# Kernel optimization log

Hardware: AMD Instinct MI355X
Metric: run time of the kernel (lower is better)

Reference implementation:

```python
import jax, jax.numpy as jnp
import numpy as np

N, E = 50000, 1600000
F_IN, F_EDGE, HID = 128, 16, 64
SLOPE = 0.2
EPS_BN = 1e-5


def setup_inputs() -> dict:
    key = jax.random.key(0)
    ks = jax.random.split(key, 24)
    g = lambda k, shp, s=0.1: (jax.random.normal(k, shp, dtype=jnp.float32) * s)
    inp = {
        'x': jax.random.normal(ks[0], (N, F_IN), dtype=jnp.float32),
        'edge_index': jax.random.randint(ks[1], (2, E), 0, N, dtype=jnp.int64),
        'edge_attr': jax.random.normal(ks[2], (E, F_EDGE), dtype=jnp.float32),
        # conv1: F_IN -> HID, 4 heads, concat
        'W1': g(ks[3], (F_IN, 4 * HID)), 'a1s': g(ks[4], (4, HID)), 'a1d': g(ks[5], (4, HID)), 'b1': jnp.zeros((4 * HID,), jnp.float32),
        # conv2: 4*HID -> HID, 4 heads, concat
        'W2': g(ks[6], (4 * HID, 4 * HID)), 'a2s': g(ks[7], (4, HID)), 'a2d': g(ks[8], (4, HID)), 'b2': jnp.zeros((4 * HID,), jnp.float32),
        # conv3: 4*HID -> HID, 1 head
        'W3': g(ks[9], (4 * HID, HID)), 'a3s': g(ks[10], (1, HID)), 'a3d': g(ks[11], (1, HID)), 'b3': jnp.zeros((HID,), jnp.float32),
        'bn1_g': jnp.ones((4 * HID,), jnp.float32), 'bn1_b': jnp.zeros((4 * HID,), jnp.float32),
        'bn2_g': jnp.ones((4 * HID,), jnp.float32), 'bn2_b': jnp.zeros((4 * HID,), jnp.float32),
        'mlp_W1': g(ks[12], (F_EDGE, HID)), 'mlp_b1': jnp.zeros((HID,), jnp.float32),
        'mlp_W2': g(ks[13], (HID, HID)), 'mlp_b2': jnp.zeros((HID,), jnp.float32),
        'fc_W': g(ks[14], (3 * HID, 1)), 'fc_b': jnp.zeros((1,), jnp.float32),
    }
    return inp


def _gat(x, W, a_s, a_d, b, src, dst, heads, dout):
    n = x.shape[0]
    h = (x @ W).reshape(n, heads, dout)                    # [N,H,D]
    ls = jnp.sum(h * a_s, axis=-1)                         # [N,H]
    ld = jnp.sum(h * a_d, axis=-1)
    logits = jax.nn.leaky_relu(ls[src] + ld[dst], SLOPE)   # [E',H]
    m = jax.ops.segment_max(logits, dst, num_segments=n)
    m = jnp.where(jnp.isfinite(m), m, 0.0)
    p = jnp.exp(logits - m[dst])
    s = jax.ops.segment_sum(p, dst, num_segments=n)
    alpha = p / (s[dst] + 1e-16)                           # segment softmax over in-edges
    out = jax.ops.segment_sum(h[src] * alpha[:, :, None], dst, num_segments=n)
    return out.reshape(n, heads * dout) + b


def _bn(x, g, b):
    mu = jnp.mean(x, axis=0)
    var = jnp.var(x, axis=0)
    return (x - mu) * jax.lax.rsqrt(var + EPS_BN) * g + b


def reference(x, edge_index, edge_attr, W1, a1s, a1d, b1, W2, a2s, a2d, b2,
              W3, a3s, a3d, b3, bn1_g, bn1_b, bn2_g, bn2_b,
              mlp_W1, mlp_b1, mlp_W2, mlp_b2, fc_W, fc_b):
    src0, dst0 = edge_index[0], edge_index[1]
    loop = jnp.arange(x.shape[0], dtype=edge_index.dtype)  # PyG adds self-loops
    src = jnp.concatenate([src0, loop])
    dst = jnp.concatenate([dst0, loop])

    h = _gat(x, W1, a1s, a1d, b1, src, dst, 4, HID)
    h = _bn(jax.nn.elu(h), bn1_g, bn1_b)
    h = _gat(h, W2, a2s, a2d, b2, src, dst, 4, HID)
    h = _bn(jax.nn.elu(h), bn2_g, bn2_b)
    h = _gat(h, W3, a3s, a3d, b3, src, dst, 1, HID)        # [N,HID]

    ef = jax.nn.relu(edge_attr @ mlp_W1 + mlp_b1) @ mlp_W2 + mlp_b2  # [E,HID]
    emb = jnp.concatenate([h[src0], h[dst0], ef], axis=1)  # [E,3*HID]
    return (emb @ fc_W + fc_b).squeeze(-1)
```

## Files before the change

### kernel.cpp

```cpp
#include <hip/hip_runtime.h>
#include <hip/hip_fp16.h>
#include <math.h>


#define FIN 128
#define HID 64
#define BIN_SHIFT 8

typedef _Float16 f16x8 __attribute__((ext_vector_type(8)));
typedef float f32x4 __attribute__((ext_vector_type(4)));

__device__ __forceinline__ unsigned short f2hbits(float f) {
    __half h = __float2half(f);
    return *reinterpret_cast<unsigned short*>(&h);
}
__device__ __forceinline__ float2 hpair(unsigned w) {
    __half2 h = *reinterpret_cast<__half2*>(&w);
    return __half22float2(h);
}

__device__ __forceinline__ unsigned fenc(float f) {
    unsigned b = __float_as_uint(f);
    return (b & 0x80000000u) ? ~b : (b | 0x80000000u);
}
__device__ __forceinline__ float fdec(unsigned k) {
    unsigned b = (k & 0x80000000u) ? (k ^ 0x80000000u) : ~k;
    return __uint_as_float(b);
}


__global__ __launch_bounds__(256) void bincount_kernel(const int* __restrict__ ei,
                                                       int* __restrict__ bincnt,
                                                       int E, int Etot) {
    __shared__ int h[256];
    int t = threadIdx.x;
    h[t] = 0;
    __syncthreads();
    int base = blockIdx.x * 4096;
    #pragma unroll
    for (int i = 0; i < 16; ++i) {
        int e = base + i * 256 + t;
        if (e < Etot) {
            int d = (e < E) ? ei[E + e] : (e - E);
            atomicAdd(&h[d >> BIN_SHIFT], 1);
        }
    }
    __syncthreads();
    if (h[t]) atomicAdd(&bincnt[t], h[t]);
}

__global__ void scanbins_kernel(const int* __restrict__ bincnt, int* __restrict__ binptr,
                                int* __restrict__ bincur, int NB, int Etot) {
    __shared__ int buf[256];
    int t = threadIdx.x;
    int v = (t < NB) ? bincnt[t] : 0;
    buf[t] = v;
    __syncthreads();
    for (int o = 1; o < 256; o <<= 1) {
        int y = (t >= o) ? buf[t - o] : 0;
        __syncthreads();
        buf[t] += y;
        __syncthreads();
    }
    int excl = buf[t] - v;
    if (t < NB) {
        binptr[t] = excl;
        bincur[t] = excl;
    }
    if (t == 0) binptr[NB] = Etot;
}

__global__ __launch_bounds__(256) void binscatter_kernel(const int* __restrict__ ei,
                                                         int* __restrict__ bincur,
                                                         int2* __restrict__ binned,
                                                         int E, int Etot) {
    __shared__ int h[256];
    __shared__ int gb[256];
    int t = threadIdx.x;
    h[t] = 0;
    __syncthreads();
    int base = blockIdx.x * 4096;
    #pragma unroll
    for (int i = 0; i < 16; ++i) {
        int e = base + i * 256 + t;
        if (e < Etot) {
            int d = (e < E) ? ei[E + e] : (e - E);
            atomicAdd(&h[d >> BIN_SHIFT], 1);
        }
    }
    __syncthreads();
    int cnt = h[t];
    if (cnt) gb[t] = atomicAdd(&bincur[t], cnt);
    __syncthreads();
    h[t] = 0;
    __syncthreads();
    #pragma unroll
    for (int i = 0; i < 16; ++i) {
        int e = base + i * 256 + t;
        if (e < Etot) {
            int s, d;
            if (e < E) { s = ei[e]; d = ei[E + e]; }
            else       { s = e - E; d = e - E; }
            int b = d >> BIN_SHIFT;
            int pos = gb[b] + atomicAdd(&h[b], 1);
            binned[pos] = make_int2(s, d);
        }
    }
}

__global__ __launch_bounds__(256) void bincsr_kernel(const int2* __restrict__ binned,
                                                     const int* __restrict__ binptr,
                                                     int* __restrict__ row_ptr,
                                                     int* __restrict__ col,
                                                     int N, int Etot) {
    __shared__ int h[256];
    __shared__ int cur[256];
    __shared__ int wsum[4];
    int b = blockIdx.x;
    int t = threadIdx.x;
    int lo = b << BIN_SHIFT;
    h[t] = 0;
    __syncthreads();
    int ebeg = binptr[b], eend = binptr[b + 1];
    for (int i = ebeg + t; i < eend; i += 256) atomicAdd(&h[binned[i].y - lo], 1);
    __syncthreads();
    int v = h[t];
    int lane = t & 63, w = t >> 6;
    int x = v;
    #pragma unroll
    for (int o = 1; o < 64; o <<= 1) {
        int y = __shfl_up(x, o);
        if (lane >= o) x += y;
    }
    if (lane == 63) wsum[w] = x;
    __syncthreads();
    int off = 0;
    #pragma unroll
    for (int i = 0; i < 4; ++i) off += (i < w) ? wsum[i] : 0;
    int excl = ebeg + off + x - v;
    int node = lo + t;
    if (node < N) row_ptr[node] = excl;
    cur[t] = excl;
    if (b == 0 && t == 0) row_ptr[N] = Etot;
    __syncthreads();
    for (int i = ebeg + t; i < eend; i += 256) {
        int2 sd = binned[i];
        int pos = atomicAdd(&cur[sd.y - lo], 1);
        col[pos] = sd.x;
    }
}


__global__ __launch_bounds__(256) void mfma_gemm_kernel(
    const float* __restrict__ X, const float* __restrict__ W,
    unsigned short* __restrict__ Yh, int Nrows, int K, int M,
    const float* __restrict__ bnsum, const float* __restrict__ bng,
    const float* __restrict__ bnb, float invN,
    const float* __restrict__ as_, const float* __restrict__ ad_,
    float* __restrict__ ls, float* __restrict__ ld,
    unsigned* __restrict__ lsmax_g, int H) {
    __shared__ __align__(16) unsigned short a_lds[128][40];
    __shared__ __align__(16) unsigned short b_lds[64][40];
    __shared__ __align__(16) float scale_l[256];
    __shared__ __align__(16) float shift_l[256];
    __shared__ unsigned lmax_l;
    const int t = threadIdx.x;
    const int nrt = (Nrows + 127) >> 7;
    int rowt, by;
    if (H == 4) {
        int idx = blockIdx.x;
        by = (idx >> 3) & 3;
        rowt = (idx & 7) + (idx >> 5) * 8;
        if (rowt >= nrt) return;
    } else {
        by = 0;
        rowt = blockIdx.x;
    }
    const int row0 = rowt * 128;
    const int c0 = by * 64;
    const int w = t >> 6, lane = t & 63;
    const int quad = lane >> 4, mrow = lane & 15;
    if (t == 0) lmax_l = 0;
    if (bnsum && t < 256) {
        float mu = bnsum[t] * invN;
        float var = bnsum[256 + t] * invN - mu * mu;
        float sc = bng[t] * rsqrtf(var + 1e-5f);
        scale_l[t] = sc;
        shift_l[t] = bnb[t] - mu * sc;
    }
    __syncthreads();
    const unsigned short* X16 = (const unsigned short*)X;
    f32x4 acc[2][4] = {};
    for (int k0 = 0; k0 < K; k0 += 32) {
        #pragma unroll
        for (int i = 0; i < 4; ++i) {
            int f = i * 256 + t;
            int r = f >> 3, kq = f & 7;
            int grow = row0 + r;
            float4 xv = make_float4(0.f, 0.f, 0.f, 0.f);
            if (bnsum) {
                uint2 hw = make_uint2(0u, 0u);
                if (grow < Nrows)
                    hw = *(const uint2*)(X16 + (size_t)grow * K + k0 + kq * 4);
                float2 f01 = hpair(hw.x), f23 = hpair(hw.y);
                xv = make_float4(f01.x, f01.y, f23.x, f23.y);
                float4 sc = *(const float4*)&scale_l[k0 + kq * 4];
                float4 sh = *(const float4*)&shift_l[k0 + kq * 4];
                xv.x = fmaf(xv.x, sc.x, sh.x);
                xv.y = fmaf(xv.y, sc.y, sh.y);
                xv.z = fmaf(xv.z, sc.z, sh.z);
                xv.w = fmaf(xv.w, sc.w, sh.w);
            } else {
                if (grow < Nrows)
                    xv = *(const float4*)(X + (size_t)grow * K + k0 + kq * 4);
            }
            ushort4 pk;
            pk.x = f2hbits(xv.x);
            pk.y = f2hbits(xv.y);
            pk.z = f2hbits(xv.z);
            pk.w = f2hbits(xv.w);
            *(ushort4*)&a_lds[r][kq * 4] = pk;
        }
        #pragma unroll
        for (int i = 0; i < 2; ++i) {
            int f = i * 256 + t;
            int kr = f >> 4, cq = f & 15;
            float4 wv = *(const float4*)(W + (size_t)(k0 + kr) * M + c0 + cq * 4);
            b_lds[cq * 4 + 0][kr] = f2hbits(wv.x);
            b_lds[cq * 4 + 1][kr] = f2hbits(wv.y);
            b_lds[cq * 4 + 2][kr] = f2hbits(wv.z);
            b_lds[cq * 4 + 3][kr] = f2hbits(wv.w);
        }
        __syncthreads();
        f16x8 a0 = *(const f16x8*)&a_lds[w * 32 + mrow][quad * 8];
        f16x8 a1 = *(const f16x8*)&a_lds[w * 32 + 16 + mrow][quad * 8];
        #pragma unroll
        for (int c = 0; c < 4; ++c) {
            f16x8 bf = *(const f16x8*)&b_lds[c * 16 + mrow][quad * 8];
            acc[0][c] = __builtin_amdgcn_mfma_f32_16x16x32_f16(a0, bf, acc[0][c], 0, 0, 0);
            acc[1][c] = __builtin_amdgcn_mfma_f32_16x16x32_f16(a1, bf, acc[1][c], 0, 0, 0);
        }
        __syncthreads();
    }
    #pragma unroll
    for (int i = 0; i < 2; ++i) {
        #pragma unroll
        for (int c = 0; c < 4; ++c) {
            #pragma unroll
            for (int r = 0; r < 4; ++r) {
                int grow = row0 + w * 32 + i * 16 + quad * 4 + r;
                if (grow < Nrows)
                    Yh[(size_t)grow * M + c0 + c * 16 + mrow] = f2hbits(acc[i][c][r]);
            }
        }
    }
    float asv[4], adv[4];
    #pragma unroll
    for (int c = 0; c < 4; ++c) {
        asv[c] = as_[by * 64 + c * 16 + mrow];
        adv[c] = ad_[by * 64 + c * 16 + mrow];
    }
    float lmax = -3.0e38f;
    #pragma unroll
    for (int i = 0; i < 2; ++i) {
        #pragma unroll
        for (int r = 0; r < 4; ++r) {
            float ps = 0.f, pd = 0.f;
            #pragma unroll
            for (int c = 0; c < 4; ++c) {
                ps = fmaf(acc[i][c][r], asv[c], ps);
                pd = fmaf(acc[i][c][r], adv[c], pd);
            }
            #pragma unroll
            for (int o = 1; o <= 8; o <<= 1) {
                ps += __shfl_xor(ps, o);
                pd += __shfl_xor(pd, o);
            }
            int grow = row0 + w * 32 + i * 16 + quad * 4 + r;
            if (mrow == 0 && grow < Nrows) {
                ls[(size_t)grow * H + by] = ps;
                ld[(size_t)grow * H + by] = pd;
                lmax = fmaxf(lmax, ps);
            }
        }
    }
    if (mrow == 0) atomicMax(&lmax_l, fenc(lmax));
    __syncthreads();
    if (t == 0) atomicMax(&lsmax_g[by], lmax_l);
}


#define ACC8(hv, p)                                              \
    {                                                            \
        float2 fa = hpair((hv).x), fb = hpair((hv).y);           \
        float2 fc = hpair((hv).z), fd = hpair((hv).w);           \
        a0 = fmaf((p), fa.x, a0); a1 = fmaf((p), fa.y, a1);      \
        a2 = fmaf((p), fb.x, a2); a3 = fmaf((p), fb.y, a3);      \
        a4 = fmaf((p), fc.x, a4); a5 = fmaf((p), fc.y, a5);      \
        a6 = fmaf((p), fd.x, a6); a7 = fmaf((p), fd.y, a7);      \
    }

__global__ __launch_bounds__(256) void agg_bn_kernel(
    const unsigned short* __restrict__ hb, const float* __restrict__ ls,
    const float* __restrict__ ld, const int* __restrict__ row_ptr,
    const int* __restrict__ col, const float* __restrict__ bias,
    const unsigned* __restrict__ lsmax_g, unsigned short* __restrict__ out,
    float* __restrict__ bnsum, int N, int ngroups) {
    __shared__ float accs[4][256];
    __shared__ float accq[4][256];
    const int t = threadIdx.x;
    const int w = t >> 6, lane = t & 63;
    const int half = lane >> 5;
    const int il = lane & 31;
    const int hd = il >> 3;
    const int c0 = il * 8;
    const char* hbb = (const char*)hb;
    const char* lsc = (const char*)ls;
    const unsigned cb = (unsigned)c0 * 2u;
    const unsigned hd4 = (unsigned)hd * 4u;
    if (half == 0) {
        #pragma unroll
        for (int i = 0; i < 8; ++i) { accs[w][c0 + i] = 0.f; accq[w][c0 + i] = 0.f; }
    }
    const float lsm = fdec(lsmax_g[hd]);
    const float4 bv0 = *(const float4*)(bias + c0);
    const float4 bv1 = *(const float4*)(bias + c0 + 4);
    for (int g = blockIdx.x; g < ngroups; g += gridDim.x) {
        int n = g * 4 + w;
        if (n >= N) continue;
        int beg = row_ptr[n], end = row_ptr[n + 1];
        float4 ldn = *(const float4*)(ld + (size_t)n * 4);
        float ldn_h = (hd == 0) ? ldn.x : (hd == 1) ? ldn.y : (hd == 2) ? ldn.z : ldn.w;
        float m_h = fmaxf(0.f, ldn_h + lsm);
        float psum = 0.f;
        float a0 = 0.f, a1 = 0.f, a2 = 0.f, a3 = 0.f;
        float a4 = 0.f, a5 = 0.f, a6 = 0.f, a7 = 0.f;
        for (int base = beg; base < end; base += 64) {
            int el = base + lane;
            int s_r = (el < end) ? col[el] : 0;
            int cnt = min(64, end - base);
            int j = 0;
            for (; j + 8 <= cnt; j += 8) {
                int s0 = __shfl(s_r, j + half);
                int s1 = __shfl(s_r, j + 2 + half);
                int s2 = __shfl(s_r, j + 4 + half);
                int s3 = __shfl(s_r, j + 6 + half);
                uint4 h0 = *(const uint4*)(hbb + ((unsigned)s0 * 512u + cb));
                uint4 h1 = *(const uint4*)(hbb + ((unsigned)s1 * 512u + cb));
                uint4 h2 = *(const uint4*)(hbb + ((unsigned)s2 * 512u + cb));
                uint4 h3 = *(const uint4*)(hbb + ((unsigned)s3 * 512u + cb));
                float l0 = *(const float*)(lsc + ((unsigned)s0 * 16u + hd4));
                float l1 = *(const float*)(lsc + ((unsigned)s1 * 16u + hd4));
                float l2 = *(const float*)(lsc + ((unsigned)s2 * 16u + hd4));
                float l3 = *(const float*)(lsc + ((unsigned)s3 * 16u + hd4));
                float g0 = l0 + ldn_h; g0 = fmaxf(g0, 0.2f * g0);
                float g1 = l1 + ldn_h; g1 = fmaxf(g1, 0.2f * g1);
                float g2 = l2 + ldn_h; g2 = fmaxf(g2, 0.2f * g2);
                float g3 = l3 + ldn_h; g3 = fmaxf(g3, 0.2f * g3);
                float p0 = __expf(g0 - m_h), p1 = __expf(g1 - m_h);
                float p2 = __expf(g2 - m_h), p3 = __expf(g3 - m_h);
                psum += (p0 + p1) + (p2 + p3);
                ACC8(h0, p0) ACC8(h1, p1) ACC8(h2, p2) ACC8(h3, p3)
            }
            for (; j < cnt; j += 2) {
                int jj = j + half;
                int sj = __shfl(s_r, jj);
                bool valid = jj < cnt;
                uint4 hv = *(const uint4*)(hbb + ((unsigned)sj * 512u + cb));
                float lv = *(const float*)(lsc + ((unsigned)sj * 16u + hd4));
                float gg = lv + ldn_h; gg = fmaxf(gg, 0.2f * gg);
                float pv = valid ? __expf(gg - m_h) : 0.f;
                psum += pv;
                ACC8(hv, pv)
            }
        }
        psum += __shfl_xor(psum, 32);
        a0 += __shfl_xor(a0, 32); a1 += __shfl_xor(a1, 32);
        a2 += __shfl_xor(a2, 32); a3 += __shfl_xor(a3, 32);
        a4 += __shfl_xor(a4, 32); a5 += __shfl_xor(a5, 32);
        a6 += __shfl_xor(a6, 32); a7 += __shfl_xor(a7, 32);
        if (half == 0) {
            float inv = 1.f / (psum + 1e-16f);
            float o0 = fmaf(a0, inv, bv0.x);
            float o1 = fmaf(a1, inv, bv0.y);
            float o2 = fmaf(a2, inv, bv0.z);
            float o3 = fmaf(a3, inv, bv0.w);
            float o4 = fmaf(a4, inv, bv1.x);
            float o5 = fmaf(a5, inv, bv1.y);
            float o6 = fmaf(a6, inv, bv1.z);
            float o7 = fmaf(a7, inv, bv1.w);
            o0 = (o0 > 0.f) ? o0 : expm1f(o0);
            o1 = (o1 > 0.f) ? o1 : expm1f(o1);
            o2 = (o2 > 0.f) ? o2 : expm1f(o2);
            o3 = (o3 > 0.f) ? o3 : expm1f(o3);
            o4 = (o4 > 0.f) ? o4 : expm1f(o4);
            o5 = (o5 > 0.f) ? o5 : expm1f(o5);
            o6 = (o6 > 0.f) ? o6 : expm1f(o6);
            o7 = (o7 > 0.f) ? o7 : expm1f(o7);
            uint4 pk;
            pk.x = (unsigned)f2hbits(o0) | ((unsigned)f2hbits(o1) << 16);
            pk.y = (unsigned)f2hbits(o2) | ((unsigned)f2hbits(o3) << 16);
            pk.z = (unsigned)f2hbits(o4) | ((unsigned)f2hbits(o5) << 16);
            pk.w = (unsigned)f2hbits(o6) | ((unsigned)f2hbits(o7) << 16);
            *(uint4*)(out + (size_t)n * 256 + c0) = pk;
            accs[w][c0 + 0] += o0; accq[w][c0 + 0] += o0 * o0;
            accs[w][c0 + 1] += o1; accq[w][c0 + 1] += o1 * o1;
            accs[w][c0 + 2] += o2; accq[w][c0 + 2] += o2 * o2;
            accs[w][c0 + 3] += o3; accq[w][c0 + 3] += o3 * o3;
            accs[w][c0 + 4] += o4; accq[w][c0 + 4] += o4 * o4;
            accs[w][c0 + 5] += o5; accq[w][c0 + 5] += o5 * o5;
            accs[w][c0 + 6] += o6; accq[w][c0 + 6] += o6 * o6;
            accs[w][c0 + 7] += o7; accq[w][c0 + 7] += o7 * o7;
        }
    }
    __syncthreads();
    float s = accs[0][t] + accs[1][t] + accs[2][t] + accs[3][t];
    float q = accq[0][t] + accq[1][t] + accq[2][t] + accq[3][t];
    atomicAdd(&bnsum[t], s);
    atomicAdd(&bnsum[256 + t], q);
}


__global__ __launch_bounds__(256) void agg3_kernel(
    const unsigned short* __restrict__ hb, const float* __restrict__ ls,
    const float* __restrict__ ld, const int* __restrict__ row_ptr,
    const int* __restrict__ col, const float* __restrict__ bias,
    const float* __restrict__ fcW, float* __restrict__ up, float* __restrict__ vp,
    const unsigned* __restrict__ lsmax_g, int N) {
    int lane = threadIdx.x & 63;
    int n = blockIdx.x * 4 + (threadIdx.x >> 6);
    if (n >= N) return;
    int beg = row_ptr[n], end = row_ptr[n + 1];
    float ldn = ld[n];
    float m_h = fmaxf(0.f, ldn + fdec(lsmax_g[0]));
    int g = lane >> 3;
    int li = lane & 7;
    int c0 = li * 8;
    const char* hbb = (const char*)hb;
    const unsigned cb = (unsigned)c0 * 2u;
    float psum = 0.f;
    float a0 = 0.f, a1 = 0.f, a2 = 0.f, a3 = 0.f;
    float a4 = 0.f, a5 = 0.f, a6 = 0.f, a7 = 0.f;
    for (int j = beg + g; j < end; j += 8) {
        int s = col[j];
        uint4 hv = *(const uint4*)(hbb + ((unsigned)s * 128u + cb));
        float lg = ls[s] + ldn;
        lg = fmaxf(lg, 0.2f * lg);
        float pv = __expf(lg - m_h);
        psum += pv;
        ACC8(hv, pv)
    }
    #pragma unroll
    for (int o = 8; o <= 32; o <<= 1) {
        psum += __shfl_xor(psum, o);
        a0 += __shfl_xor(a0, o); a1 += __shfl_xor(a1, o);
        a2 += __shfl_xor(a2, o); a3 += __shfl_xor(a3, o);
        a4 += __shfl_xor(a4, o); a5 += __shfl_xor(a5, o);
        a6 += __shfl_xor(a6, o); a7 += __shfl_xor(a7, o);
    }
    float inv = 1.f / (psum + 1e-16f);
    float v0 = fmaf(a0, inv, bias[c0 + 0]);
    float v1 = fmaf(a1, inv, bias[c0 + 1]);
    float v2 = fmaf(a2, inv, bias[c0 + 2]);
    float v3 = fmaf(a3, inv, bias[c0 + 3]);
    float v4 = fmaf(a4, inv, bias[c0 + 4]);
    float v5 = fmaf(a5, inv, bias[c0 + 5]);
    float v6 = fmaf(a6, inv, bias[c0 + 6]);
    float v7 = fmaf(a7, inv, bias[c0 + 7]);
    float pu = v0 * fcW[c0] + v1 * fcW[c0 + 1] + v2 * fcW[c0 + 2] + v3 * fcW[c0 + 3] +
               v4 * fcW[c0 + 4] + v5 * fcW[c0 + 5] + v6 * fcW[c0 + 6] + v7 * fcW[c0 + 7];
    float pv2 = v0 * fcW[64 + c0] + v1 * fcW[64 + c0 + 1] + v2 * fcW[64 + c0 + 2] +
                v3 * fcW[64 + c0 + 3] + v4 * fcW[64 + c0 + 4] + v5 * fcW[64 + c0 + 5] +
                v6 * fcW[64 + c0 + 6] + v7 * fcW[64 + c0 + 7];
    #pragma unroll
    for (int o = 1; o <= 4; o <<= 1) {
        pu += __shfl_xor(pu, o);
        pv2 += __shfl_xor(pv2, o);
    }
    if (lane == 0) {
        up[n] = pu;
        vp[n] = pv2;
    }
}


__global__ __launch_bounds__(256) void edge_out_kernel(
    const int* __restrict__ ei, const float* __restrict__ ea,
    const float* __restrict__ W1, const float* __restrict__ b1,
    const float* __restrict__ mlpW2, const float* __restrict__ mlpb2,
    const float* __restrict__ fcW, const float* __restrict__ fcb,
    const float* __restrict__ u, const float* __restrict__ v,
    float* __restrict__ out, int E) {
    __shared__ __align__(16) float W1T[64][16];
    __shared__ float w2fl[64];
    __shared__ float b1l[64];
    __shared__ float c2l;
    int t = threadIdx.x;
    for (int p = t; p < 1024; p += 256) {
        int i = p >> 6, j = p & 63;
        W1T[j][i] = W1[i * 64 + j];
    }
    if (t < 64) {
        float s = 0.f;
        for (int k = 0; k < 64; ++k) s = fmaf(mlpW2[t * 64 + k], fcW[128 + k], s);
        w2fl[t] = s;
        b1l[t] = b1[t];
    }
    if (t == 0) {
        float c = fcb[0];
        for (int k = 0; k < 64; ++k) c = fmaf(mlpb2[k], fcW[128 + k], c);
        c2l = c;
    }
    __syncthreads();
    int base = blockIdx.x * 1024;
    float eav[4][16];
    int sidx[4], didx[4];
    bool ok[4];
    #pragma unroll
    for (int k = 0; k < 4; ++k) {
        int e = base + k * 256 + t;
        ok[k] = e < E;
        int ec = ok[k] ? e : 0;
        sidx[k] = ei[ec];
        didx[k] = ei[E + ec];
        const float4* ear = (const float4*)(ea + (size_t)ec * 16);
        float4 q0 = ear[0], q1 = ear[1], q2 = ear[2], q3 = ear[3];
        eav[k][0] = q0.x;  eav[k][1] = q0.y;  eav[k][2] = q0.z;  eav[k][3] = q0.w;
        eav[k][4] = q1.x;  eav[k][5] = q1.y;  eav[k][6] = q1.z;  eav[k][7] = q1.w;
        eav[k][8] = q2.x;  eav[k][9] = q2.y;  eav[k][10] = q2.z; eav[k][11] = q2.w;
        eav[k][12] = q3.x; eav[k][13] = q3.y; eav[k][14] = q3.z; eav[k][15] = q3.w;
    }
    float acc[4] = {0.f, 0.f, 0.f, 0.f};
    #pragma unroll 4
    for (int j = 0; j < 64; ++j) {
        const float4* wr = (const float4*)&W1T[j][0];
        float4 w0 = wr[0], w1 = wr[1], w2 = wr[2], w3 = wr[3];
        float wrow[16] = {w0.x, w0.y, w0.z, w0.w, w1.x, w1.y, w1.z, w1.w,
                          w2.x, w2.y, w2.z, w2.w, w3.x, w3.y, w3.z, w3.w};
        float bj = b1l[j], wj = w2fl[j];
        #pragma unroll
        for (int k = 0; k < 4; ++k) {
            float s = bj;
            #pragma unroll
            for (int q = 0; q < 16; ++q) s = fmaf(eav[k][q], wrow[q], s);
            s = fmaxf(s, 0.f);
            acc[k] = fmaf(s, wj, acc[k]);
        }
    }
    float cc = c2l;
    #pragma unroll
    for (int k = 0; k < 4; ++k) {
        if (ok[k]) {
            int e = base + k * 256 + t;
            out[e] = u[sidx[k]] + v[didx[k]] + acc[k] + cc;
        }
    }
}


extern "C" void kernel_launch(void* const* d_in, const int* in_sizes, int n_in,
                              void* d_out, int out_size, void* d_ws, size_t ws_size,
                              hipStream_t stream) {
    const float* x     = (const float*)d_in[0];
    const int*   ei    = (const int*)d_in[1];
    const float* ea    = (const float*)d_in[2];
    const float* W1    = (const float*)d_in[3];
    const float* a1s   = (const float*)d_in[4];
    const float* a1d   = (const float*)d_in[5];
    const float* b1    = (const float*)d_in[6];
    const float* W2    = (const float*)d_in[7];
    const float* a2s   = (const float*)d_in[8];
    const float* a2d   = (const float*)d_in[9];
    const float* b2    = (const float*)d_in[10];
    const float* W3    = (const float*)d_in[11];
    const float* a3s   = (const float*)d_in[12];
    const float* a3d   = (const float*)d_in[13];
    const float* b3    = (const float*)d_in[14];
    const float* bn1g  = (const float*)d_in[15];
    const float* bn1b  = (const float*)d_in[16];
    const float* bn2g  = (const float*)d_in[17];
    const float* bn2b  = (const float*)d_in[18];
    const float* mlpW1 = (const float*)d_in[19];
    const float* mlpb1 = (const float*)d_in[20];
    const float* mlpW2 = (const float*)d_in[21];
    const float* mlpb2 = (const float*)d_in[22];
    const float* fcW   = (const float*)d_in[23];
    const float* fcb   = (const float*)d_in[24];
    float* out = (float*)d_out;

    const int N = in_sizes[0] / FIN;
    const int E = in_sizes[1] / 2;
    const int Etot = E + N;
    const int NB = (N + 255) >> BIN_SHIFT;

    char* wsb = (char*)d_ws;
    size_t off = 0;
    auto alloc = [&](size_t bytes) {
        void* p = wsb + off;
        off += (bytes + 63) & ~(size_t)63;
        return p;
    };
    unsigned short* hAb = (unsigned short*)alloc((size_t)N * 256 * 2);
    unsigned short* hB  = (unsigned short*)alloc((size_t)N * 256 * 2);
    unsigned short* h3b = (unsigned short*)alloc((size_t)N * 64 * 2);
    float* lsb = (float*)alloc((size_t)N * 4 * 4);
    float* ldb = (float*)alloc((size_t)N * 4 * 4);
    int* row_ptr = (int*)alloc((size_t)(N + 1) * 4);
    int* colb    = (int*)alloc((size_t)Etot * 4);
    int2* binned = (int2*)alloc((size_t)Etot * 8);
    int* zreg    = (int*)alloc((256 + 16 + 512 + 512) * 4);
    int* bincnt  = zreg;
    unsigned* lsmax1 = (unsigned*)(zreg + 256);
    unsigned* lsmax2 = lsmax1 + 4;
    unsigned* lsmax3 = lsmax1 + 8;
    float* bnsumA = (float*)(zreg + 256 + 16);
    float* bnsumB = bnsumA + 512;
    int* binptr  = (int*)alloc((size_t)(NB + 1) * 4);
    int* bincur  = (int*)alloc((size_t)NB * 4);
    float* ub  = (float*)alloc((size_t)N * 4);
    float* vb  = (float*)alloc((size_t)N * 4);
    (void)ws_size; (void)n_in; (void)out_size;

    const int nb4 = (N + 3) / 4;
    const int nch = (Etot + 4095) / 4096;
    const float invN = 1.f / (float)N;
    const int nrt = (N + 127) / 128;
    const int g4 = ((nrt + 7) / 8) * 32;

    hipMemsetAsync(zreg, 0, (256 + 16 + 512 + 512) * sizeof(int), stream);
    bincount_kernel<<<nch, 256, 0, stream>>>(ei, bincnt, E, Etot);
    scanbins_kernel<<<1, 256, 0, stream>>>(bincnt, binptr, bincur, NB, Etot);
    binscatter_kernel<<<nch, 256, 0, stream>>>(ei, bincur, binned, E, Etot);
    bincsr_kernel<<<NB, 256, 0, stream>>>(binned, binptr, row_ptr, colb, N, Etot);

    mfma_gemm_kernel<<<g4, 256, 0, stream>>>(x, W1, hAb, N, 128, 256,
        nullptr, nullptr, nullptr, invN, a1s, a1d, lsb, ldb, lsmax1, 4);
    agg_bn_kernel<<<2048, 256, 0, stream>>>(hAb, lsb, ldb, row_ptr, colb, b1,
                                            lsmax1, hB, bnsumA, N, nb4);
    mfma_gemm_kernel<<<g4, 256, 0, stream>>>((const float*)hB, W2, hAb, N, 256, 256,
        bnsumA, bn1g, bn1b, invN, a2s, a2d, lsb, ldb, lsmax2, 4);
    agg_bn_kernel<<<2048, 256, 0, stream>>>(hAb, lsb, ldb, row_ptr, colb, b2,
                                            lsmax2, hB, bnsumB, N, nb4);
    mfma_gemm_kernel<<<nrt, 256, 0, stream>>>((const float*)hB, W3, h3b, N, 256, 64,
        bnsumB, bn2g, bn2b, invN, a3s, a3d, lsb, ldb, lsmax3, 1);
    agg3_kernel<<<nb4, 256, 0, stream>>>(h3b, lsb, ldb, row_ptr, colb, b3,
                                         fcW, ub, vb, lsmax3, N);
    edge_out_kernel<<<(E + 1023) / 1024, 256, 0, stream>>>(
        ei, ea, mlpW1, mlpb1, mlpW2, mlpb2, fcW, fcb, ub, vb, out, E);
}
```

Baseline: 753.9 us.

## Use MFMA fp16 for edge MLP and reuse shared-atomic ranks in binscatter

The edge MLP first layer (16->64 plus ReLU and a dot with the folded second layer) moves from per-thread scalar FMAs to 16x16x32 fp16 MFMA tiles, with edge attributes converted to half and reduced across lanes by shuffles. The kernel becomes a grid-stride loop over 2048 blocks. Binscatter also keeps each edge's rank from the first shared-memory atomic pass, dropping the second atomic pass and one barrier. The fp16 conversion of inputs and weights lowers precision, and half of the MFMA K dimension is zero padding.

```diff
diff --git a/kernel.cpp b/kernel.cpp
--- a/kernel.cpp
+++ b/kernel.cpp
@@ -80,19 +80,18 @@
     h[t] = 0;
     __syncthreads();
     int base = blockIdx.x * 4096;
+    int lp[16];
     #pragma unroll
     for (int i = 0; i < 16; ++i) {
         int e = base + i * 256 + t;
         if (e < Etot) {
             int d = (e < E) ? ei[E + e] : (e - E);
-            atomicAdd(&h[d >> BIN_SHIFT], 1);
+            lp[i] = atomicAdd(&h[d >> BIN_SHIFT], 1);
         }
     }
     __syncthreads();
     int cnt = h[t];
     if (cnt) gb[t] = atomicAdd(&bincur[t], cnt);
-    __syncthreads();
-    h[t] = 0;
     __syncthreads();
     #pragma unroll
     for (int i = 0; i < 16; ++i) {
@@ -102,8 +101,7 @@
             if (e < E) { s = ei[e]; d = ei[E + e]; }
             else       { s = e - E; d = e - E; }
             int b = d >> BIN_SHIFT;
-            int pos = gb[b] + atomicAdd(&h[b], 1);
-            binned[pos] = make_int2(s, d);
+            binned[gb[b] + lp[i]] = make_int2(s, d);
         }
     }
 }
@@ -491,15 +489,13 @@
     const float* __restrict__ fcW, const float* __restrict__ fcb,
     const float* __restrict__ u, const float* __restrict__ v,
     float* __restrict__ out, int E) {
-    __shared__ __align__(16) float W1T[64][16];
+    __shared__ __align__(16) unsigned short W1h[16][64];
     __shared__ float w2fl[64];
     __shared__ float b1l[64];
     __shared__ float c2l;
     int t = threadIdx.x;
-    for (int p = t; p < 1024; p += 256) {
-        int i = p >> 6, j = p & 63;
-        W1T[j][i] = W1[i * 64 + j];
-    }
+    for (int p = t; p < 1024; p += 256)
+        W1h[p >> 6][p & 63] = f2hbits(W1[p]);
     if (t < 64) {
         float s = 0.f;
         for (int k = 0; k < 64; ++k) s = fmaf(mlpW2[t * 64 + k], fcW[128 + k], s);
@@ -512,47 +508,62 @@
         c2l = c;
     }
     __syncthreads();
-    int base = blockIdx.x * 1024;
-    float eav[4][16];
-    int sidx[4], didx[4];
-    bool ok[4];
-    #pragma unroll
-    for (int k = 0; k < 4; ++k) {
-        int e = base + k * 256 + t;
-        ok[k] = e < E;
-        int ec = ok[k] ? e : 0;
-        sidx[k] = ei[ec];
-        didx[k] = ei[E + ec];
-        const float4* ear = (const float4*)(ea + (size_t)ec * 16);
-        float4 q0 = ear[0], q1 = ear[1], q2 = ear[2], q3 = ear[3];
-        eav[k][0] = q0.x;  eav[k][1] = q0.y;  eav[k][2] = q0.z;  eav[k][3] = q0.w;
-        eav[k][4] = q1.x;  eav[k][5] = q1.y;  eav[k][6] = q1.z;  eav[k][7] = q1.w;
-        eav[k][8] = q2.x;  eav[k][9] = q2.y;  eav[k][10] = q2.z; eav[k][11] = q2.w;
-        eav[k][12] = q3.x; eav[k][13] = q3.y; eav[k][14] = q3.z; eav[k][15] = q3.w;
-    }
-    float acc[4] = {0.f, 0.f, 0.f, 0.f};
-    #pragma unroll 4
-    for (int j = 0; j < 64; ++j) {
-        const float4* wr = (const float4*)&W1T[j][0];
-        float4 w0 = wr[0], w1 = wr[1], w2 = wr[2], w3 = wr[3];
-        float wrow[16] = {w0.x, w0.y, w0.z, w0.w, w1.x, w1.y, w1.z, w1.w,
-                          w2.x, w2.y, w2.z, w2.w, w3.x, w3.y, w3.z, w3.w};
-        float bj = b1l[j], wj = w2fl[j];
-        #pragma unroll
-        for (int k = 0; k < 4; ++k) {
-            float s = bj;
+    const int w = t >> 6, lane = t & 63;
+    const int col = lane & 15, kq = lane >> 4;
+    f16x8 bf[4];
+    float b1c[4], wjc[4];
+    #pragma unroll
+    for (int c = 0; c < 4; ++c) {
+        unsigned short tmp[8];
+        #pragma unroll
+        for (int i = 0; i < 8; ++i)
+            tmp[i] = (kq < 2) ? W1h[kq * 8 + i][c * 16 + col] : (unsigned short)0;
+        bf[c] = *(const f16x8*)tmp;
+        b1c[c] = b1l[c * 16 + col];
+        wjc[c] = w2fl[c * 16 + col];
+    }
+    const float cc = c2l;
+    const int E16 = (E + 15) >> 4;
+    const int gw = blockIdx.x * 4 + w;
+    const int nw = gridDim.x * 4;
+    for (int g = gw; g < E16; g += nw) {
+        int e0 = g << 4;
+        int edge = e0 + col;
+        f16x8 af;
+        if (kq < 2 && edge < E) {
+            const float4* ap = (const float4*)(ea + (size_t)edge * 16 + kq * 8);
+            float4 x0 = ap[0], x1 = ap[1];
+            unsigned short tmp[8] = {f2hbits(x0.x), f2hbits(x0.y), f2hbits(x0.z),
+                                     f2hbits(x0.w), f2hbits(x1.x), f2hbits(x1.y),
+                                     f2hbits(x1.z), f2hbits(x1.w)};
+            af = *(const f16x8*)tmp;
+        } else {
+            unsigned short z[8] = {0, 0, 0, 0, 0, 0, 0, 0};
+            af = *(const f16x8*)z;
+        }
+        f32x4 zz = {};
+        f32x4 d0 = __builtin_amdgcn_mfma_f32_16x16x32_f16(af, bf[0], zz, 0, 0, 0);
+        f32x4 d1 = __builtin_amdgcn_mfma_f32_16x16x32_f16(af, bf[1], zz, 0, 0, 0);
+        f32x4 d2 = __builtin_amdgcn_mfma_f32_16x16x32_f16(af, bf[2], zz, 0, 0, 0);
+        f32x4 d3 = __builtin_amdgcn_mfma_f32_16x16x32_f16(af, bf[3], zz, 0, 0, 0);
+        float sr[4];
+        #pragma unroll
+        for (int r = 0; r < 4; ++r) {
+            float q0 = fmaxf(d0[r] + b1c[0], 0.f);
+            float q1 = fmaxf(d1[r] + b1c[1], 0.f);
+            float q2 = fmaxf(d2[r] + b1c[2], 0.f);
+            float q3 = fmaxf(d3[r] + b1c[3], 0.f);
+            float acc = q0 * wjc[0] + q1 * wjc[1] + q2 * wjc[2] + q3 * wjc[3];
             #pragma unroll
-            for (int q = 0; q < 16; ++q) s = fmaf(eav[k][q], wrow[q], s);
-            s = fmaxf(s, 0.f);
-            acc[k] = fmaf(s, wj, acc[k]);
-        }
-    }
-    float cc = c2l;
-    #pragma unroll
-    for (int k = 0; k < 4; ++k) {
-        if (ok[k]) {
-            int e = base + k * 256 + t;
-            out[e] = u[sidx[k]] + v[didx[k]] + acc[k] + cc;
+            for (int o = 1; o <= 8; o <<= 1) acc += __shfl_xor(acc, o);
+            sr[r] = acc;
+        }
+        if (col < 4) {
+            int e = e0 + kq * 4 + col;
+            if (e < E) {
+                int si = ei[e], di = ei[E + e];
+                out[e] = u[si] + v[di] + sr[col] + cc;
+            }
         }
     }
 }
@@ -645,6 +656,6 @@
         bnsumB, bn2g, bn2b, invN, a3s, a3d, lsb, ldb, lsmax3, 1);
     agg3_kernel<<<nb4, 256, 0, stream>>>(h3b, lsb, ldb, row_ptr, colb, b3,
                                          fcW, ub, vb, lsmax3, N);
-    edge_out_kernel<<<(E + 1023) / 1024, 256, 0, stream>>>(
+    edge_out_kernel<<<2048, 256, 0, stream>>>(
         ei, ea, mlpW1, mlpb1, mlpW2, mlpb2, fcW, fcb, ub, vb, out, E);
 }
```

After: 758.1 us. Within noise of the previous version (+0.6%).
